# Kernel optimization log

Hardware: AMD Instinct MI355X
Metric: run time of the kernel (lower is better)

Reference implementation:

```python
import jax, jax.numpy as jnp
import numpy as np

B, S, H, NH, PF, L, V = 8, 1024, 1024, 16, 4096, 6, 32000
HD = H // NH
STD = 0.02
NEG = -1e10


def setup_inputs() -> dict:
    key = jax.random.key(0)
    ks = jax.random.split(key, 12)
    inp = {
        "src": jax.random.randint(ks[0], (B, S), 0, V),
        "src_mask": jnp.ones((B, 1, 1, S), dtype=bool),
        "tok_emb": jax.random.normal(ks[1], (V, H), jnp.float32) * STD,
        "pos_emb": jax.random.normal(ks[2], (S, H), jnp.float32) * STD,
        "Wq": jax.random.normal(ks[3], (L, H, H), jnp.float32) * STD,
        "bq": jnp.zeros((L, H), jnp.float32),
        "Wk": jax.random.normal(ks[4], (L, H, H), jnp.float32) * STD,
        "bk": jnp.zeros((L, H), jnp.float32),
        "Wv": jax.random.normal(ks[5], (L, H, H), jnp.float32) * STD,
        "bv": jnp.zeros((L, H), jnp.float32),
        "Wo": jax.random.normal(ks[6], (L, H, H), jnp.float32) * STD,
        "bo": jnp.zeros((L, H), jnp.float32),
        "W1": jax.random.normal(ks[7], (L, H, PF), jnp.float32) * STD,
        "b1": jnp.zeros((L, PF), jnp.float32),
        "W2": jax.random.normal(ks[8], (L, PF, H), jnp.float32) * STD,
        "b2": jnp.zeros((L, H), jnp.float32),
        "ln1_g": jnp.ones((L, H), jnp.float32),
        "ln1_b": jnp.zeros((L, H), jnp.float32),
        "ln2_g": jnp.ones((L, H), jnp.float32),
        "ln2_b": jnp.zeros((L, H), jnp.float32),
    }
    return inp


def layer_norm(x, g, b, eps=1e-5):
    m = jnp.mean(x, axis=-1, keepdims=True)
    v = jnp.mean((x - m) ** 2, axis=-1, keepdims=True)
    return (x - m) * jax.lax.rsqrt(v + eps) * g + b


def reference(src, src_mask, tok_emb, pos_emb, Wq, bq, Wk, bk, Wv, bv, Wo, bo,
              W1, b1, W2, b2, ln1_g, ln1_b, ln2_g, ln2_b):
    # embedding * sqrt(hid_dim) + positional embedding (dropout = identity at eval)
    x = tok_emb[src] * jnp.sqrt(jnp.float32(H)) + pos_emb[None, :S]
    attn_scale = jnp.sqrt(jnp.float32(HD))
    for l in range(L):
        # multi-head self-attention
        q = (x @ Wq[l] + bq[l]).reshape(B, S, NH, HD).transpose(0, 2, 1, 3)
        k = (x @ Wk[l] + bk[l]).reshape(B, S, NH, HD).transpose(0, 2, 1, 3)
        v = (x @ Wv[l] + bv[l]).reshape(B, S, NH, HD).transpose(0, 2, 1, 3)
        energy = jnp.einsum('bhqd,bhkd->bhqk', q, k) / attn_scale  # [B,NH,S,S]
        energy = jnp.where(src_mask, energy, NEG)
        attn = jax.nn.softmax(energy, axis=-1)
        o = jnp.einsum('bhqk,bhkd->bhqd', attn, v)
        o = o.transpose(0, 2, 1, 3).reshape(B, S, H) @ Wo[l] + bo[l]
        x = layer_norm(x + o, ln1_g[l], ln1_b[l])
        # position-wise feedforward
        f = jax.nn.relu(x @ W1[l] + b1[l]) @ W2[l] + b2[l]
        x = layer_norm(x + f, ln2_g[l], ln2_b[l])
    return x
```

## Files before the change

kernel.cpp:

```cpp
#include <hip/hip_runtime.h>
#include <cstdint>
#include <cstddef>


#define DI __device__ __forceinline__

typedef __attribute__((ext_vector_type(8))) short short8;
typedef __attribute__((ext_vector_type(4))) short s16x4;
typedef __attribute__((ext_vector_type(4))) float f32x4;
typedef __attribute__((ext_vector_type(4))) unsigned u32x4;

static constexpr int H  = 1024;
static constexpr int S  = 1024;
static constexpr int BB = 8;
static constexpr int NH = 16;
static constexpr int PF = 4096;
static constexpr int M  = BB * S;
static constexpr int L  = 6;

DI short f2bf(float f) {
  unsigned u = __builtin_bit_cast(unsigned, f);
  u += 0x7fffu + ((u >> 16) & 1u);
  return (short)(u >> 16);
}

DI unsigned packbf(float a, float b) {
  return (__builtin_bit_cast(unsigned, a) >> 16) |
         (__builtin_bit_cast(unsigned, b) & 0xffff0000u);
}

DI void async16(void* lds, const void* g) {
  __builtin_amdgcn_global_load_lds(
      (const __attribute__((address_space(1))) unsigned*)g,
      (__attribute__((address_space(3))) unsigned*)lds, 16, 0, 0);
}

DI f32x4 mfma16(short8 a, short8 b, f32x4 c) {
  return __builtin_amdgcn_mfma_f32_16x16x32_bf16(a, b, c, 0, 0, 0);
}

__global__ __launch_bounds__(256) void embed_kernel(
    const int* __restrict__ src, const float* __restrict__ tok,
    const float* __restrict__ pos, float* __restrict__ xf,
    short* __restrict__ xb) {
  const int row = blockIdx.x;
  const int s = row & (S - 1);
  const int i0 = threadIdx.x << 2;
  const int v = src[row];
  const float4 te = *(const float4*)(tok + (size_t)v * H + i0);
  const float4 pe = *(const float4*)(pos + (size_t)s * H + i0);
  float o[4] = {te.x * 32.f + pe.x, te.y * 32.f + pe.y,
                te.z * 32.f + pe.z, te.w * 32.f + pe.w};
  *(float4*)(xf + (size_t)row * H + i0) = make_float4(o[0], o[1], o[2], o[3]);
  s16x4 pk;
  pk[0] = f2bf(o[0]); pk[1] = f2bf(o[1]); pk[2] = f2bf(o[2]); pk[3] = f2bf(o[3]);
  *(s16x4*)(xb + (size_t)row * H + i0) = pk;
}

__global__ __launch_bounds__(256) void wconv_kernel(
    const float* __restrict__ W, short* __restrict__ Wt, int K, int N) {
  __shared__ float tile[64][65];
  const int ntn = N >> 6;
  const int k0 = (blockIdx.x / ntn) << 6;
  const int n0 = (blockIdx.x % ntn) << 6;
  const int r4 = threadIdx.x >> 6, cc = threadIdx.x & 63;
#pragma unroll
  for (int i = 0; i < 16; i++) {
    const int r = (i << 2) + r4;
    tile[r][cc] = W[(size_t)(k0 + r) * N + n0 + cc];
  }
  __syncthreads();
#pragma unroll
  for (int i = 0; i < 16; i++) {
    const int n = (i << 2) + r4;
    Wt[(size_t)(n0 + n) * K + k0 + cc] = f2bf(tile[cc][n]);
  }
}

template <int MREP, int EPI>
__global__ __launch_bounds__(512, 2) void gemm256(
    const short* __restrict__ A, const short* __restrict__ Bt,
    const float* __restrict__ bias, void* __restrict__ out,
    const int N, const int K) {
  constexpr int WM = 16 / MREP;
  constexpr int WN = 8 / WM;
  constexpr int BN = WN * 64;
  constexpr int P  = MREP / 2;
  constexpr int BL = BN / 64;
  extern __shared__ char lds[];
  short* lA = (short*)lds;
  short* lB = (short*)(lds + 65536);

  const int tid = threadIdx.x;
  const int w = tid >> 6, lane = tid & 63;
  const int g = lane >> 4, ci = lane & 15;
  const int wm = w / WN, wn = w % WN;

  const int nwg = gridDim.x;
  const int bid = (int)blockIdx.x;
  const int swz = (bid & 7) * (nwg >> 3) + (bid >> 3);
  const int bm = swz & 31, bn = swz >> 5;
  const int brow = bm << 8;
  const int bcol = bn * BN;

  const int srow = lane >> 3;
  const int schk = (lane & 7) ^ srow;
  const short* aS[4];
#pragma unroll
  for (int j = 0; j < 4; j++)
    aS[j] = A + (size_t)(brow + w * 8 + j * 64 + srow) * K + schk * 8;
  const short* bS[BL];
#pragma unroll
  for (int j = 0; j < BL; j++)
    bS[j] = Bt + (size_t)(bcol + w * 8 + j * 64 + srow) * K + schk * 8;

  int aoff[2], boff[2];
#pragma unroll
  for (int ks = 0; ks < 2; ks++) {
    aoff[ks] = (wm * MREP * 16 + ci) * 128 + (((ks * 4 + g) ^ (ci & 7)) << 4);
    boff[ks] = (wn * 64 + ci) * 128 + (((ks * 4 + g) ^ (ci & 7)) << 4);
  }

  f32x4 acc[MREP][4];
#pragma unroll
  for (int i = 0; i < MREP; i++)
#pragma unroll
    for (int j = 0; j < 4; j++) acc[i][j] = f32x4{0.f, 0.f, 0.f, 0.f};

  auto stage = [&](int kt, int buf) {
    short* la = lA + buf * (256 * 64);
    short* lb = lB + buf * (BN * 64);
    const int ko = kt << 6;
#pragma unroll
    for (int j = 0; j < 4; j++)
      async16(la + (w * 64 + j * 512) * 8, aS[j] + ko);
#pragma unroll
    for (int j = 0; j < BL; j++)
      async16(lb + (w * 64 + j * 512) * 8, bS[j] + ko);
  };

  stage(0, 0);
  stage(1, 1);
  if constexpr (BL == 4) asm volatile("s_waitcnt vmcnt(8)" ::: "memory");
  else                   asm volatile("s_waitcnt vmcnt(6)" ::: "memory");
  __builtin_amdgcn_sched_barrier(0);
  __builtin_amdgcn_s_barrier();

  const int nt = K >> 6;
  short8 bfr[4];
  for (int t = 0; t < nt; t++) {
    const int cur = t & 1;
    const char* la = (const char*)(lA + cur * (256 * 64));
    const char* lb = (const char*)(lB + cur * (BN * 64));
#pragma unroll
    for (int p = 0; p < P; p++) {
      const int ks = (MREP == 8) ? (p >> 1) : p;
      const int h  = (MREP == 8) ? (p & 1) : 0;
      short8 afr[4];
#pragma unroll
      for (int mi = 0; mi < 4; mi++)
        afr[mi] = *(const short8*)(la + aoff[ks] + (h * 4 + mi) * 2048);
      if (h == 0) {
#pragma unroll
        for (int ni = 0; ni < 4; ni++)
          bfr[ni] = *(const short8*)(lb + boff[ks] + ni * 2048);
      }
      __builtin_amdgcn_s_barrier();
      asm volatile("s_waitcnt lgkmcnt(0)" ::: "memory");
      __builtin_amdgcn_sched_barrier(0);
      __builtin_amdgcn_s_setprio(1);
#pragma unroll
      for (int mi = 0; mi < 4; mi++)
#pragma unroll
        for (int ni = 0; ni < 4; ni++)
          acc[h * 4 + mi][ni] = mfma16(afr[mi], bfr[ni], acc[h * 4 + mi][ni]);
      __builtin_amdgcn_s_setprio(0);
      if (p + 1 < P) __builtin_amdgcn_s_barrier();
    }
    if (t + 1 == nt) break;
    __builtin_amdgcn_s_barrier();
    if (t + 2 < nt) {
      stage(t + 2, cur);
      if constexpr (BL == 4) asm volatile("s_waitcnt vmcnt(8)" ::: "memory");
      else                   asm volatile("s_waitcnt vmcnt(6)" ::: "memory");
    } else {
      asm volatile("s_waitcnt vmcnt(0)" ::: "memory");
    }
    __builtin_amdgcn_sched_barrier(0);
    __builtin_amdgcn_s_barrier();
  }

#pragma unroll
  for (int ni = 0; ni < 4; ni++) {
    const int col = bcol + wn * 64 + ni * 16 + ci;
    const float bv = bias[col];
#pragma unroll
    for (int mi = 0; mi < MREP; mi++) {
      const int row0 = brow + wm * (MREP * 16) + mi * 16 + (g << 2);
      if constexpr (EPI == 0 || EPI == 1) {
        short* o = (short*)out;
#pragma unroll
        for (int r = 0; r < 4; r++) {
          float vv = acc[mi][ni][r] + bv;
          if constexpr (EPI == 1) vv = fmaxf(vv, 0.f);
          o[(size_t)(row0 + r) * N + col] = f2bf(vv);
        }
      } else if constexpr (EPI == 2) {
        float* o = (float*)out;
#pragma unroll
        for (int r = 0; r < 4; r++)
          o[(size_t)(row0 + r) * N + col] = acc[mi][ni][r] + bv;
      } else {
        short* o = (short*)out;
        const int bidx = row0 >> 10, s0 = row0 & (S - 1);
        s16x4 pk;
#pragma unroll
        for (int r = 0; r < 4; r++) pk[r] = f2bf(acc[mi][ni][r] + bv);
        *(s16x4*)(o + ((size_t)bidx * H + col) * S + s0) = pk;
      }
    }
  }
}

__global__ __launch_bounds__(256) void attn_kernel(
    const short* __restrict__ q, const short* __restrict__ k,
    const short* __restrict__ vt, short* __restrict__ ao) {
  __shared__ short lsk[2][4096];
  __shared__ short lsv[2][4096];
  const int tid = threadIdx.x;
  const int w = tid >> 6, lane = tid & 63;
  const int g = lane >> 4, ci = lane & 15;
  const int bid = ((int)blockIdx.x & 7) * 256 + ((int)blockIdx.x >> 3);
  const int qt = bid & 15;
  const int bh = bid >> 4;
  const int b = bh >> 4, h = bh & 15;
  const int hbase = h << 6;

  const int r8 = lane >> 3, c8 = lane & 7;
  const int cs = c8 ^ r8;
  const short* kbase = k + ((size_t)b * S) * H + hbase;
  const short* vbase = vt + ((size_t)b * H + hbase) * S;

  const size_t qrow = (size_t)b * S + (qt << 6) + (w << 4) + ci;
  short8 qf[2];
#pragma unroll
  for (int ks = 0; ks < 2; ks++)
    qf[ks] = *(const short8*)(q + qrow * H + hbase + ks * 32 + (g << 3));

  const int swz = ci & 7;
  int koff[2], voff[2][2];
#pragma unroll
  for (int ks = 0; ks < 2; ks++) {
    koff[ks] = ci * 128 + (((4 * ks + g) ^ swz) << 4);
#pragma unroll
    for (int pc = 0; pc < 2; pc++)
      voff[ks][pc] =
          ci * 128 + (((4 * ks + 2 * pc + (g >> 1)) ^ swz) << 4) + ((g & 1) << 3);
  }

#pragma unroll
  for (int t = 0; t < 2; t++) {
    const int row = (w << 3) + t * 32 + r8;
    async16(&lsk[0][t * 2048 + (w << 9)], kbase + (size_t)row * H + cs * 8);
    async16(&lsv[0][t * 2048 + (w << 9)], vbase + (size_t)row * S + cs * 8);
  }
  __syncthreads();

  const f32x4 zero = {0.f, 0.f, 0.f, 0.f};
  f32x4 of[4];
#pragma unroll
  for (int nf = 0; nf < 4; nf++) of[nf] = zero;
  float mrun = -INFINITY, lsum = 0.f;

#pragma unroll 2
  for (int kt = 0; kt < 16; kt++) {
    const int cur = kt & 1;
    if (kt < 15) {
      const int kr1 = (kt + 1) << 6;
#pragma unroll
      for (int t = 0; t < 2; t++) {
        const int row = (w << 3) + t * 32 + r8;
        async16(&lsk[cur ^ 1][t * 2048 + (w << 9)],
                kbase + (size_t)(kr1 + row) * H + cs * 8);
        async16(&lsv[cur ^ 1][t * 2048 + (w << 9)],
                vbase + (size_t)row * S + kr1 + cs * 8);
      }
    }
    const char* kb = (const char*)lsk[cur];
    const char* vb = (const char*)lsv[cur];

    f32x4 st[4];
#pragma unroll
    for (int mf = 0; mf < 4; mf++) st[mf] = zero;
#pragma unroll
    for (int ks = 0; ks < 2; ks++)
#pragma unroll
      for (int mf = 0; mf < 4; mf++) {
        const short8 kf = *(const short8*)(kb + koff[ks] + mf * 2048);
        st[mf] = mfma16(kf, qf[ks], st[mf]);
      }

    float tmax = -INFINITY;
#pragma unroll
    for (int mf = 0; mf < 4; mf++)
#pragma unroll
      for (int r = 0; r < 4; r++) tmax = fmaxf(tmax, st[mf][r]);
    tmax = fmaxf(tmax, __shfl_xor(tmax, 16));
    tmax = fmaxf(tmax, __shfl_xor(tmax, 32));
    const float mnew = fmaxf(mrun, tmax * 0.125f);
    const float alpha = __expf(mrun - mnew);
    float rs = 0.f;
    float p[4][4];
#pragma unroll
    for (int mf = 0; mf < 4; mf++)
#pragma unroll
      for (int r = 0; r < 4; r++) {
        p[mf][r] = __expf(__builtin_fmaf(st[mf][r], 0.125f, -mnew));
        rs += p[mf][r];
      }
    rs += __shfl_xor(rs, 16);
    rs += __shfl_xor(rs, 32);
    lsum = lsum * alpha + rs;
    mrun = mnew;

    unsigned pk[4][2];
#pragma unroll
    for (int mf = 0; mf < 4; mf++) {
      pk[mf][0] = packbf(p[mf][0], p[mf][1]);
      pk[mf][1] = packbf(p[mf][2], p[mf][3]);
    }
#pragma unroll
    for (int nf = 0; nf < 4; nf++)
#pragma unroll
      for (int r = 0; r < 4; r++) of[nf][r] *= alpha;

#pragma unroll
    for (int ks = 0; ks < 2; ks++) {
      u32x4 uu;
      uu[0] = pk[2 * ks][0];
      uu[1] = pk[2 * ks][1];
      uu[2] = pk[2 * ks + 1][0];
      uu[3] = pk[2 * ks + 1][1];
      const short8 pfrag = __builtin_bit_cast(short8, uu);
#pragma unroll
      for (int nf = 0; nf < 4; nf++) {
        union { short8 v8; s16x4 h[2]; } vv;
        vv.h[0] = *(const s16x4*)(vb + voff[ks][0] + nf * 2048);
        vv.h[1] = *(const s16x4*)(vb + voff[ks][1] + nf * 2048);
        of[nf] = mfma16(vv.v8, pfrag, of[nf]);
      }
    }
    __syncthreads();
  }

  const float inv = 1.f / lsum;
#pragma unroll
  for (int nf = 0; nf < 4; nf++) {
    s16x4 o4;
#pragma unroll
    for (int r = 0; r < 4; r++) o4[r] = f2bf(of[nf][r] * inv);
    *(s16x4*)(ao + qrow * H + hbase + (nf << 4) + (g << 2)) = o4;
  }
}

__global__ __launch_bounds__(256) void ln_kernel(
    const float* __restrict__ x, const float* __restrict__ t,
    const float* __restrict__ gm, const float* __restrict__ bt,
    float* __restrict__ yf, short* __restrict__ yb) {
  const int row = blockIdx.x;
  const int i0 = threadIdx.x << 2;
  const size_t base = (size_t)row * H + i0;
  const float4 a = *(const float4*)(x + base);
  const float4 bb = *(const float4*)(t + base);
  float v[4] = {a.x + bb.x, a.y + bb.y, a.z + bb.z, a.w + bb.w};
  float s = v[0] + v[1] + v[2] + v[3];
  float qq = v[0] * v[0] + v[1] * v[1] + v[2] * v[2] + v[3] * v[3];
#pragma unroll
  for (int off = 32; off; off >>= 1) {
    s += __shfl_down(s, off);
    qq += __shfl_down(qq, off);
  }
  __shared__ float red[8];
  const int w = threadIdx.x >> 6, lane = threadIdx.x & 63;
  if (lane == 0) { red[w] = s; red[4 + w] = qq; }
  __syncthreads();
  s = red[0] + red[1] + red[2] + red[3];
  qq = red[4] + red[5] + red[6] + red[7];
  const float mean = s * (1.f / H);
  float var = qq * (1.f / H) - mean * mean;
  var = fmaxf(var, 0.f);
  const float rstd = rsqrtf(var + 1e-5f);
  const float4 gv = *(const float4*)(gm + i0);
  const float4 bv = *(const float4*)(bt + i0);
  float y[4] = {(v[0] - mean) * rstd * gv.x + bv.x,
                (v[1] - mean) * rstd * gv.y + bv.y,
                (v[2] - mean) * rstd * gv.z + bv.z,
                (v[3] - mean) * rstd * gv.w + bv.w};
  *(float4*)(yf + base) = make_float4(y[0], y[1], y[2], y[3]);
  s16x4 pk;
  pk[0] = f2bf(y[0]); pk[1] = f2bf(y[1]); pk[2] = f2bf(y[2]); pk[3] = f2bf(y[3]);
  *(s16x4*)(yb + base) = pk;
}

extern "C" void kernel_launch(void* const* d_in, const int* in_sizes, int n_in,
                              void* d_out, int out_size, void* d_ws, size_t ws_size,
                              hipStream_t stream) {
  const int* src = (const int*)d_in[0];
  const float* tok = (const float*)d_in[2];
  const float* pos = (const float*)d_in[3];
  const float* Wq = (const float*)d_in[4];
  const float* bq = (const float*)d_in[5];
  const float* Wk = (const float*)d_in[6];
  const float* bk = (const float*)d_in[7];
  const float* Wv = (const float*)d_in[8];
  const float* bv = (const float*)d_in[9];
  const float* Wo = (const float*)d_in[10];
  const float* bo = (const float*)d_in[11];
  const float* W1 = (const float*)d_in[12];
  const float* b1 = (const float*)d_in[13];
  const float* W2 = (const float*)d_in[14];
  const float* b2 = (const float*)d_in[15];
  const float* g1 = (const float*)d_in[16];
  const float* be1 = (const float*)d_in[17];
  const float* g2 = (const float*)d_in[18];
  const float* be2 = (const float*)d_in[19];

  hipFuncSetAttribute(reinterpret_cast<const void*>(gemm256<8, 1>),
                      hipFuncAttributeMaxDynamicSharedMemorySize, 131072);
  hipFuncSetAttribute(reinterpret_cast<const void*>(gemm256<4, 0>),
                      hipFuncAttributeMaxDynamicSharedMemorySize, 98304);
  hipFuncSetAttribute(reinterpret_cast<const void*>(gemm256<4, 2>),
                      hipFuncAttributeMaxDynamicSharedMemorySize, 98304);
  hipFuncSetAttribute(reinterpret_cast<const void*>(gemm256<4, 3>),
                      hipFuncAttributeMaxDynamicSharedMemorySize, 98304);

  char* p = (char*)d_ws;
  auto take = [&](size_t bytes) {
    char* r = p;
    p += (bytes + 255) & ~(size_t)255;
    return r;
  };
  float* xf   = (float*)take((size_t)M * H * 4);
  short* xb   = (short*)take((size_t)M * H * 2);
  float* tmp  = (float*)take((size_t)M * H * 4);
  short* qb   = (short*)take((size_t)M * H * 2);
  short* kbuf = (short*)take((size_t)M * H * 2);
  short* vtb  = (short*)take((size_t)M * H * 2);
  short* aob  = (short*)take((size_t)M * H * 2);
  short* fb   = (short*)take((size_t)M * PF * 2);
  short* wtq  = (short*)take((size_t)H * H * 2);
  short* wtk  = (short*)take((size_t)H * H * 2);
  short* wtv  = (short*)take((size_t)H * H * 2);
  short* wto  = (short*)take((size_t)H * H * 2);
  short* wt1  = (short*)take((size_t)H * PF * 2);
  short* wt2  = (short*)take((size_t)H * PF * 2);

  embed_kernel<<<M, 256, 0, stream>>>(src, tok, pos, xf, xb);

  for (int l = 0; l < L; l++) {
    wconv_kernel<<<(H / 64) * (H / 64), 256, 0, stream>>>(Wq + (size_t)l * H * H, wtq, H, H);
    wconv_kernel<<<(H / 64) * (H / 64), 256, 0, stream>>>(Wk + (size_t)l * H * H, wtk, H, H);
    wconv_kernel<<<(H / 64) * (H / 64), 256, 0, stream>>>(Wv + (size_t)l * H * H, wtv, H, H);
    wconv_kernel<<<(H / 64) * (H / 64), 256, 0, stream>>>(Wo + (size_t)l * H * H, wto, H, H);
    wconv_kernel<<<(H / 64) * (PF / 64), 256, 0, stream>>>(W1 + (size_t)l * H * PF, wt1, H, PF);
    wconv_kernel<<<(PF / 64) * (H / 64), 256, 0, stream>>>(W2 + (size_t)l * PF * H, wt2, PF, H);

    gemm256<4, 0><<<256, 512, 98304, stream>>>(xb, wtq, bq + (size_t)l * H, qb, H, H);
    gemm256<4, 0><<<256, 512, 98304, stream>>>(xb, wtk, bk + (size_t)l * H, kbuf, H, H);
    gemm256<4, 3><<<256, 512, 98304, stream>>>(xb, wtv, bv + (size_t)l * H, vtb, H, H);
    attn_kernel<<<BB * NH * (S / 64), 256, 0, stream>>>(qb, kbuf, vtb, aob);
    gemm256<4, 2><<<256, 512, 98304, stream>>>(aob, wto, bo + (size_t)l * H, tmp, H, H);
    ln_kernel<<<M, 256, 0, stream>>>(xf, tmp, g1 + (size_t)l * H, be1 + (size_t)l * H, xf, xb);
    gemm256<8, 1><<<512, 512, 131072, stream>>>(xb, wt1, b1 + (size_t)l * PF, fb, PF, H);
    gemm256<4, 2><<<256, 512, 98304, stream>>>(fb, wt2, b2 + (size_t)l * H, tmp, H, PF);
    float* yf = (l == L - 1) ? (float*)d_out : xf;
    ln_kernel<<<M, 256, 0, stream>>>(xf, tmp, g2 + (size_t)l * H, be2 + (size_t)l * H, yf, xb);
  }
}
```

Measured before the change: 2.449 ms.

## Switch GEMM to 4-slot BK=32 ring pipeline with XCD-aware tile mapping

Restructures the main GEMM mainloop from a double-buffered BK=64 scheme to a 4-slot ring of BK=32 stages, prefetching three stages ahead and interleaving the async loads between MFMA phases. The block-to-tile mapping is changed so that each XCD covers a contiguous group of M and N tiles, aiming for better L2 reuse. The transposed-V epilogue now stages results through LDS and writes coalesced 16-byte stores, and the row-major epilogue is reordered so each row's columns are written together. The risks are more barriers per K step and more complex vmcnt bookkeeping, and the new tile mapping assumes a 32-tile M grid.

```diff
diff --git a/kernel.cpp b/kernel.cpp
--- a/kernel.cpp
+++ b/kernel.cpp
@@ -85,86 +85,98 @@
   constexpr int WM = 16 / MREP;
   constexpr int WN = 8 / WM;
   constexpr int BN = WN * 64;
-  constexpr int P  = MREP / 2;
-  constexpr int BL = BN / 64;
+  constexpr int BLB = BN / 128;
+  constexpr int LPH = 2 + BLB;
+  constexpr int SLOT = (256 + BN) * 32 * 2;
   extern __shared__ char lds[];
-  short* lA = (short*)lds;
-  short* lB = (short*)(lds + 65536);
 
   const int tid = threadIdx.x;
   const int w = tid >> 6, lane = tid & 63;
   const int g = lane >> 4, ci = lane & 15;
   const int wm = w / WN, wn = w % WN;
 
-  const int nwg = gridDim.x;
+  const int nbn = N / BN;
   const int bid = (int)blockIdx.x;
-  const int swz = (bid & 7) * (nwg >> 3) + (bid >> 3);
-  const int bm = swz & 31, bn = swz >> 5;
+  const int xcd = bid & 7, i = bid >> 3;
+  const int bm = ((xcd & 3) << 3) | (i & 7);
+  const int bn = (xcd >> 2) * (nbn >> 1) + (i >> 3);
   const int brow = bm << 8;
   const int bcol = bn * BN;
 
-  const int srow = lane >> 3;
-  const int schk = (lane & 7) ^ srow;
-  const short* aS[4];
-#pragma unroll
-  for (int j = 0; j < 4; j++)
-    aS[j] = A + (size_t)(brow + w * 8 + j * 64 + srow) * K + schk * 8;
-  const short* bS[BL];
-#pragma unroll
-  for (int j = 0; j < BL; j++)
-    bS[j] = Bt + (size_t)(bcol + w * 8 + j * 64 + srow) * K + schk * 8;
-
-  int aoff[2], boff[2];
-#pragma unroll
-  for (int ks = 0; ks < 2; ks++) {
-    aoff[ks] = (wm * MREP * 16 + ci) * 128 + (((ks * 4 + g) ^ (ci & 7)) << 4);
-    boff[ks] = (wn * 64 + ci) * 128 + (((ks * 4 + g) ^ (ci & 7)) << 4);
-  }
+  const int srow = lane >> 2;
+  const int schk = (lane & 3) ^ (srow & 3);
+  const short* aS[2];
+#pragma unroll
+  for (int j = 0; j < 2; j++)
+    aS[j] = A + (size_t)(brow + w * 16 + j * 128 + srow) * K + schk * 8;
+  const short* bS[BLB];
+#pragma unroll
+  for (int j = 0; j < BLB; j++)
+    bS[j] = Bt + (size_t)(bcol + w * 16 + j * 128 + srow) * K + schk * 8;
+
+  const int aoff = (wm * (MREP * 16) + ci) * 64 + ((g ^ (ci & 3)) << 4);
+  const int boff = (wn * 64 + ci) * 64 + ((g ^ (ci & 3)) << 4);
+
+  auto stageP = [&](int hh, int part) {
+    char* sa = lds + (hh & 3) * SLOT;
+    char* sb = sa + 16384;
+    const int ko = hh << 5;
+    if constexpr (MREP == 8) {
+      async16(sa + (w * 64 + part * 512) * 16, aS[part] + ko);
+      async16(sb + (w * 64 + part * 512) * 16, bS[part] + ko);
+    } else {
+      async16(sa + (w * 64) * 16, aS[0] + ko);
+      async16(sa + (w * 64 + 512) * 16, aS[1] + ko);
+      async16(sb + (w * 64) * 16, bS[0] + ko);
+    }
+  };
+  auto stageAll = [&](int hh) {
+    if constexpr (MREP == 8) { stageP(hh, 0); stageP(hh, 1); }
+    else stageP(hh, 0);
+  };
 
   f32x4 acc[MREP][4];
 #pragma unroll
-  for (int i = 0; i < MREP; i++)
-#pragma unroll
-    for (int j = 0; j < 4; j++) acc[i][j] = f32x4{0.f, 0.f, 0.f, 0.f};
-
-  auto stage = [&](int kt, int buf) {
-    short* la = lA + buf * (256 * 64);
-    short* lb = lB + buf * (BN * 64);
-    const int ko = kt << 6;
-#pragma unroll
-    for (int j = 0; j < 4; j++)
-      async16(la + (w * 64 + j * 512) * 8, aS[j] + ko);
-#pragma unroll
-    for (int j = 0; j < BL; j++)
-      async16(lb + (w * 64 + j * 512) * 8, bS[j] + ko);
-  };
-
-  stage(0, 0);
-  stage(1, 1);
-  if constexpr (BL == 4) asm volatile("s_waitcnt vmcnt(8)" ::: "memory");
-  else                   asm volatile("s_waitcnt vmcnt(6)" ::: "memory");
+  for (int a = 0; a < MREP; a++)
+#pragma unroll
+    for (int b = 0; b < 4; b++) acc[a][b] = f32x4{0.f, 0.f, 0.f, 0.f};
+
+  stageAll(0); stageAll(1); stageAll(2);
+  if constexpr (MREP == 8) asm volatile("s_waitcnt vmcnt(8)" ::: "memory");
+  else                     asm volatile("s_waitcnt vmcnt(6)" ::: "memory");
   __builtin_amdgcn_sched_barrier(0);
   __builtin_amdgcn_s_barrier();
 
-  const int nt = K >> 6;
-  short8 bfr[4];
-  for (int t = 0; t < nt; t++) {
-    const int cur = t & 1;
-    const char* la = (const char*)(lA + cur * (256 * 64));
-    const char* lb = (const char*)(lB + cur * (BN * 64));
-#pragma unroll
-    for (int p = 0; p < P; p++) {
-      const int ks = (MREP == 8) ? (p >> 1) : p;
-      const int h  = (MREP == 8) ? (p & 1) : 0;
-      short8 afr[4];
+  const int nt2 = K >> 5;
+  for (int h = 0; h < nt2; h++) {
+    const char* la = lds + (h & 3) * SLOT;
+    const char* lb = la + 16384;
+    const bool pf = (h + 3 < nt2);
+    short8 bfr[4], afr[4];
+#pragma unroll
+    for (int ni = 0; ni < 4; ni++)
+      bfr[ni] = *(const short8*)(lb + boff + ni * 1024);
+#pragma unroll
+    for (int mi = 0; mi < 4; mi++)
+      afr[mi] = *(const short8*)(la + aoff + mi * 1024);
+    if (pf) stageP(h + 3, 0);
+    __builtin_amdgcn_s_barrier();
+    asm volatile("s_waitcnt lgkmcnt(0)" ::: "memory");
+    __builtin_amdgcn_sched_barrier(0);
+    __builtin_amdgcn_s_setprio(1);
+#pragma unroll
+    for (int mi = 0; mi < 4; mi++)
+#pragma unroll
+      for (int ni = 0; ni < 4; ni++)
+        acc[mi][ni] = mfma16(afr[mi], bfr[ni], acc[mi][ni]);
+    __builtin_amdgcn_s_setprio(0);
+    if constexpr (MREP == 8) {
+      __builtin_amdgcn_s_barrier();
+      short8 af2[4];
 #pragma unroll
       for (int mi = 0; mi < 4; mi++)
-        afr[mi] = *(const short8*)(la + aoff[ks] + (h * 4 + mi) * 2048);
-      if (h == 0) {
-#pragma unroll
-        for (int ni = 0; ni < 4; ni++)
-          bfr[ni] = *(const short8*)(lb + boff[ks] + ni * 2048);
-      }
+        af2[mi] = *(const short8*)(la + aoff + (4 + mi) * 1024);
+      if (pf) stageP(h + 3, 1);
       __builtin_amdgcn_s_barrier();
       asm volatile("s_waitcnt lgkmcnt(0)" ::: "memory");
       __builtin_amdgcn_sched_barrier(0);
@@ -173,16 +185,15 @@
       for (int mi = 0; mi < 4; mi++)
 #pragma unroll
         for (int ni = 0; ni < 4; ni++)
-          acc[h * 4 + mi][ni] = mfma16(afr[mi], bfr[ni], acc[h * 4 + mi][ni]);
+          acc[4 + mi][ni] = mfma16(af2[mi], bfr[ni], acc[4 + mi][ni]);
       __builtin_amdgcn_s_setprio(0);
-      if (p + 1 < P) __builtin_amdgcn_s_barrier();
-    }
-    if (t + 1 == nt) break;
-    __builtin_amdgcn_s_barrier();
-    if (t + 2 < nt) {
-      stage(t + 2, cur);
-      if constexpr (BL == 4) asm volatile("s_waitcnt vmcnt(8)" ::: "memory");
-      else                   asm volatile("s_waitcnt vmcnt(6)" ::: "memory");
+    }
+    if (h + 4 <= nt2) {
+      if constexpr (MREP == 8) asm volatile("s_waitcnt vmcnt(8)" ::: "memory");
+      else                     asm volatile("s_waitcnt vmcnt(6)" ::: "memory");
+    } else if (h + 3 == nt2) {
+      if constexpr (MREP == 8) asm volatile("s_waitcnt vmcnt(4)" ::: "memory");
+      else                     asm volatile("s_waitcnt vmcnt(3)" ::: "memory");
     } else {
       asm volatile("s_waitcnt vmcnt(0)" ::: "memory");
     }
@@ -190,34 +201,51 @@
     __builtin_amdgcn_s_barrier();
   }
 
-#pragma unroll
-  for (int ni = 0; ni < 4; ni++) {
-    const int col = bcol + wn * 64 + ni * 16 + ci;
-    const float bv = bias[col];
+  if constexpr (EPI <= 2) {
 #pragma unroll
     for (int mi = 0; mi < MREP; mi++) {
-      const int row0 = brow + wm * (MREP * 16) + mi * 16 + (g << 2);
-      if constexpr (EPI == 0 || EPI == 1) {
-        short* o = (short*)out;
-#pragma unroll
-        for (int r = 0; r < 4; r++) {
-          float vv = acc[mi][ni][r] + bv;
+      float bv[4];
+#pragma unroll
+      for (int ni = 0; ni < 4; ni++)
+        bv[ni] = bias[bcol + wn * 64 + ni * 16 + ci];
+#pragma unroll
+      for (int r = 0; r < 4; r++) {
+        const int row = brow + wm * (MREP * 16) + mi * 16 + (g << 2) + r;
+#pragma unroll
+        for (int ni = 0; ni < 4; ni++) {
+          const int col = bcol + wn * 64 + ni * 16 + ci;
+          float vv = acc[mi][ni][r] + bv[ni];
           if constexpr (EPI == 1) vv = fmaxf(vv, 0.f);
-          o[(size_t)(row0 + r) * N + col] = f2bf(vv);
+          if constexpr (EPI == 2) ((float*)out)[(size_t)row * N + col] = vv;
+          else ((short*)out)[(size_t)row * N + col] = f2bf(vv);
         }
-      } else if constexpr (EPI == 2) {
-        float* o = (float*)out;
-#pragma unroll
-        for (int r = 0; r < 4; r++)
-          o[(size_t)(row0 + r) * N + col] = acc[mi][ni][r] + bv;
-      } else {
-        short* o = (short*)out;
-        const int bidx = row0 >> 10, s0 = row0 & (S - 1);
+      }
+    }
+  } else {
+    __syncthreads();
+    short* t = (short*)lds;
+#pragma unroll
+    for (int ni = 0; ni < 4; ni++) {
+      const int d = wn * 64 + ni * 16 + ci;
+      const float bv = bias[bcol + d];
+#pragma unroll
+      for (int mi = 0; mi < 4; mi++) {
+        const int s0 = wm * 64 + mi * 16 + (g << 2);
         s16x4 pk;
 #pragma unroll
         for (int r = 0; r < 4; r++) pk[r] = f2bf(acc[mi][ni][r] + bv);
-        *(s16x4*)(o + ((size_t)bidx * H + col) * S + s0) = pk;
+        *(s16x4*)(t + d * 264 + s0) = pk;
       }
+    }
+    __syncthreads();
+    const int b = brow >> 10;
+    short* o = (short*)out;
+#pragma unroll
+    for (int rr = 0; rr < 8; rr++) {
+      const int c = tid + rr * 512;
+      const int d = c >> 5, sc = c & 31;
+      const short8 v = *(const short8*)(t + d * 264 + sc * 8);
+      *(short8*)(o + ((size_t)b * H + bcol + d) * S + (brow & (S - 1)) + sc * 8) = v;
     }
   }
 }
```

Result: faster. 2.326 ms (-5.0%).
